# Performance work log

Measured on AMD Instinct MI355X. Metric: run time of the kernel, lower is better.

## Reference

```python
import jax, jax.numpy as jnp
import numpy as np

B, T, C = 256, 256, 147
BPM, H_DIM, NH = 32, 64, 4
HD = H_DIM // NH


def setup_inputs() -> dict:
    key = jax.random.key(0)
    ks = jax.random.split(key, 12)
    def lin(k, fan_in, fan_out):
        bound = 1.0 / np.sqrt(fan_in)
        kw, kb = jax.random.split(k)
        W = jax.random.uniform(kw, (fan_in, fan_out), jnp.float32, -bound, bound)
        b = jax.random.uniform(kb, (fan_out,), jnp.float32, -bound, bound)
        return W, b
    Wq, bq = lin(ks[0], C, H_DIM)
    Wk, bk = lin(ks[1], C, H_DIM)
    Wv, bv = lin(ks[2], C, H_DIM)
    Wb, bb = lin(ks[3], BPM, H_DIM)
    Wo, bo = lin(ks[4], H_DIM, C)
    pose = jax.random.normal(ks[5], (B, T, C), jnp.float32)
    bpm_emb = jax.random.normal(ks[6], (B, BPM), jnp.float32)
    return {"pose": pose, "bpm_emb": bpm_emb,
            "Wq": Wq, "bq": bq, "Wk": Wk, "bk": bk, "Wv": Wv, "bv": bv,
            "Wb": Wb, "bb": bb, "Wo": Wo, "bo": bo}


def reference(pose, bpm_emb, Wq, bq, Wk, bk, Wv, bv, Wb, bb, Wo, bo):
    Bb, Tt, Cc = pose.shape
    scale = HD ** -0.5
    # projections -> [B, H, T, hd]
    def split_heads(x):
        return x.reshape(Bb, Tt, NH, HD).transpose(0, 2, 1, 3)
    q = split_heads(pose @ Wq + bq)
    k = split_heads(pose @ Wk + bk)
    v = split_heads(pose @ Wv + bv)
    # bpm-conditioned key bias: [B, H, 1, hd]
    bpm_feat = (bpm_emb @ Wb + bb).reshape(Bb, 1, NH, HD).transpose(0, 2, 1, 3)
    k = k + bpm_feat
    # attention
    scores = jnp.einsum('bhqd,bhkd->bhqk', q, k) * scale
    attn = jax.nn.softmax(scores, axis=-1)
    out = jnp.einsum('bhqk,bhkd->bhqd', attn, v)
    out = out.transpose(0, 2, 1, 3).reshape(Bb, Tt, NH * HD)
    return out @ Wo + bo
```

## Files before the change

### kernel.cpp

```cpp
#include <hip/hip_runtime.h>

constexpr int kC = 147, kH = 64, kHD = 16, kBPM = 32;

typedef __attribute__((ext_vector_type(8)))  short bf16x8;
typedef __attribute__((ext_vector_type(4)))  float f32x4;
typedef __attribute__((ext_vector_type(16))) float f32x16;
typedef __attribute__((ext_vector_type(4)))  short s16x4;

__device__ __forceinline__ short f2bf(float f) {
    unsigned u = __builtin_bit_cast(unsigned, f);
    u += 0x7fffu + ((u >> 16) & 1u);
    return (short)(u >> 16);
}
#define MFMA16(a,b,c) __builtin_amdgcn_mfma_f32_16x16x32_bf16((a),(b),(c),0,0,0)
#define MFMA32(a,b,c) __builtin_amdgcn_mfma_f32_32x32x16_bf16((a),(b),(c),0,0,0)

#if __has_builtin(__builtin_amdgcn_exp2f)
  #define EXP2(x) __builtin_amdgcn_exp2f(x)
#else
  #define EXP2(x) __expf((x) * 0.6931471805599453f)
#endif
constexpr float kQScale = 0.25f * 1.4426950408889634f;

constexpr int QS  = 72;
constexpr int VS  = 264;
constexpr int PS  = 40;
constexpr int WSS = 168;
constexpr int WOS = 72;

__device__ __forceinline__ void stage_w_qkv(const float* __restrict__ W,
                                            float scale, short* Ws, int tid) {
    #pragma unroll
    for (int it = 0; it < 5; ++it) {
        const int i = it * 1024 + tid;
        const int c = i & 63, k = (i >> 6) * 2;
        const float v0 = (k     < kC) ? W[k * kH + c] * scale : 0.f;
        const float v1 = (k + 1 < kC) ? W[(k + 1) * kH + c] * scale : 0.f;
        const unsigned pack = (unsigned)(unsigned short)f2bf(v0)
                            | ((unsigned)(unsigned short)f2bf(v1) << 16);
        *(unsigned*)&Ws[c * WSS + (k ^ (((c >> 3) & 3) << 3))] = pack;
    }
}

__global__ __launch_bounds__(1024, 4) void fused_kernel(
    const float* __restrict__ pose, const float* __restrict__ bpm_emb,
    const float* __restrict__ Wq, const float* __restrict__ bq,
    const float* __restrict__ Wk, const float* __restrict__ bk,
    const float* __restrict__ Wv, const float* __restrict__ bv,
    const float* __restrict__ Wb, const float* __restrict__ bb,
    const float* __restrict__ Wo, const float* __restrict__ bo,
    float* __restrict__ out)
{
    __shared__ __align__(16) short qs[256 * QS];
    __shared__ __align__(16) short ks_[256 * QS];
    __shared__ __align__(16) short vt[kH * VS];
    __shared__ __align__(16) short WsPt[20480];
    __shared__ float l_s[16 * 64];
    __shared__ float bias_s[192];
    short* const Ws = WsPt;
    short* const Pt = WsPt;

    const int tid = threadIdx.x;
    const int w = tid >> 6, lane = tid & 63;
    const int ll = lane & 15, lq = lane >> 4;
    const int lm = lane & 31, lh = lane >> 5;
    const int b = blockIdx.x;
    const size_t pbase = (size_t)b * 256 * kC;

    bf16x8 pf[5];
    {
        const int row = w * 16 + ll;
        const float* prow = pose + pbase + (size_t)row * kC;
        #pragma unroll
        for (int ksp = 0; ksp < 5; ++ksp) {
            const int c0 = ksp * 32 + lq * 8;
            float v[8];
            if (c0 + 8 <= kC) {
                const float4 f0 = *(const float4*)(prow + c0);
                const float4 f1 = *(const float4*)(prow + c0 + 4);
                v[0]=f0.x; v[1]=f0.y; v[2]=f0.z; v[3]=f0.w;
                v[4]=f1.x; v[5]=f1.y; v[6]=f1.z; v[7]=f1.w;
            } else {
                #pragma unroll
                for (int e = 0; e < 8; ++e) v[e] = (c0 + e < kC) ? prow[c0 + e] : 0.f;
            }
            bf16x8 t;
            #pragma unroll
            for (int e = 0; e < 8; ++e) t[e] = f2bf(v[e]);
            pf[ksp] = t;
        }
    }
    if (tid < 192) {
        const int m = tid >> 6, c = tid & 63;
        float a = ((m == 0) ? bq : (m == 1) ? bk : bv)[c];
        if (m == 1) {
            a += bb[c];
            #pragma unroll
            for (int k2 = 0; k2 < kBPM; ++k2)
                a = fmaf(bpm_emb[b * kBPM + k2], Wb[k2 * kH + c], a);
        }
        if (m == 0) a *= kQScale;
        bias_s[tid] = a;
    }
    stage_w_qkv(Wq, kQScale, Ws, tid);
    __syncthreads();

    for (int m = 0; m < 3; ++m) {
        f32x4 acc[4];
        #pragma unroll
        for (int mt = 0; mt < 4; ++mt) acc[mt] = (f32x4){0.f,0.f,0.f,0.f};
        #pragma unroll
        for (int ksp = 0; ksp < 5; ++ksp)
            #pragma unroll
            for (int mt = 0; mt < 4; ++mt) {
                const int c = mt * 16 + ll;
                const int key = ((c >> 3) & 3) << 3;
                const bf16x8 wf = *(const bf16x8*)(Ws + c * WSS + ((ksp*32 + lq*8) ^ key));
                acc[mt] = MFMA16(wf, pf[ksp], acc[mt]);
            }
        __syncthreads();
        if (m == 0)      stage_w_qkv(Wk, 1.0f, Ws, tid);
        else if (m == 1) stage_w_qkv(Wv, 1.0f, Ws, tid);
        const int row = w * 16 + ll;
        #pragma unroll
        for (int mt = 0; mt < 4; ++mt) {
            const int c0 = mt * 16 + 4 * lq;
            const float4 bv4 = *(const float4*)&bias_s[m * kH + c0];
            if (m < 2) {
                s16x4 pk;
                pk[0] = f2bf(acc[mt][0] + bv4.x);
                pk[1] = f2bf(acc[mt][1] + bv4.y);
                pk[2] = f2bf(acc[mt][2] + bv4.z);
                pk[3] = f2bf(acc[mt][3] + bv4.w);
                *(s16x4*)((m == 0 ? qs : ks_) + row * QS + c0) = pk;
            } else {
                vt[(c0 + 0) * VS + row] = f2bf(acc[mt][0] + bv4.x);
                vt[(c0 + 1) * VS + row] = f2bf(acc[mt][1] + bv4.y);
                vt[(c0 + 2) * VS + row] = f2bf(acc[mt][2] + bv4.z);
                vt[(c0 + 3) * VS + row] = f2bf(acc[mt][3] + bv4.w);
            }
        }
        __syncthreads();
    }

    const int h = w & 3;
    const int q0 = (w >> 2) * 64;
    bf16x8 qf[2];
    #pragma unroll
    for (int s32 = 0; s32 < 2; ++s32)
        qf[s32] = *(const bf16x8*)(qs + (q0 + s32*32 + lm) * QS + h*16 + lh*8);

    f32x4 oacc[2][2];
    #pragma unroll
    for (int s32 = 0; s32 < 2; ++s32) {
        oacc[s32][0] = (f32x4){0.f,0.f,0.f,0.f};
        oacc[s32][1] = (f32x4){0.f,0.f,0.f,0.f};
    }
    float lp[2] = {0.f, 0.f};
    short* Pw = Pt + w * 32 * PS;
    const int wkey = ((lm >> 3) & 3) << 3;

    for (int jb = 0; jb < 8; ++jb) {
        const int j0 = jb * 32;
        const bf16x8 kf = *(const bf16x8*)(ks_ + (j0 + lm) * QS + h*16 + lh*8);
        const bf16x8 vf = *(const bf16x8*)(vt + (h*16 + ll) * VS + j0 + lq*8);
        #pragma unroll
        for (int s32 = 0; s32 < 2; ++s32) {
            const f32x16 z16 = {0.f,0.f,0.f,0.f,0.f,0.f,0.f,0.f,
                                0.f,0.f,0.f,0.f,0.f,0.f,0.f,0.f};
            const f32x16 s = MFMA32(kf, qf[s32], z16);
            float sum = 0.f;
            #pragma unroll
            for (int g = 0; g < 4; ++g) {
                const float p0 = EXP2(s[4*g + 0]);
                const float p1 = EXP2(s[4*g + 1]);
                const float p2 = EXP2(s[4*g + 2]);
                const float p3 = EXP2(s[4*g + 3]);
                sum += (p0 + p1) + (p2 + p3);
                s16x4 pk; pk[0] = f2bf(p0); pk[1] = f2bf(p1);
                pk[2] = f2bf(p2); pk[3] = f2bf(p3);
                *(s16x4*)(Pw + lm * PS + ((8*g + 4*lh) ^ wkey)) = pk;
            }
            lp[s32] += sum;
            #pragma unroll
            for (int half = 0; half < 2; ++half) {
                const int qp = half * 16 + ll;
                const int rkey = ((qp >> 3) & 3) << 3;
                const bf16x8 pfr = *(const bf16x8*)(Pw + qp * PS + ((lq*8) ^ rkey));
                oacc[s32][half] = MFMA16(vf, pfr, oacc[s32][half]);
            }
        }
    }
    #pragma unroll
    for (int s32 = 0; s32 < 2; ++s32) {
        const float l2 = lp[s32] + __shfl_xor(lp[s32], 32);
        if (lane < 32) l_s[w * 64 + s32 * 32 + lm] = l2;
    }
    #pragma unroll
    for (int s32 = 0; s32 < 2; ++s32)
        #pragma unroll
        for (int half = 0; half < 2; ++half) {
            const int qi = s32 * 32 + half * 16 + ll;
            const float inv = 1.f / l_s[w * 64 + qi];
            s16x4 pk;
            #pragma unroll
            for (int r = 0; r < 4; ++r) pk[r] = f2bf(oacc[s32][half][r] * inv);
            *(s16x4*)(qs + (q0 + qi) * QS + h*16 + 4*lq) = pk;
        }
    __syncthreads();

    #pragma unroll
    for (int it = 0; it < 5; ++it) {
        const int i = it * 1024 + tid;
        const int n = i % 160, k = (i / 160) * 2;
        const float v0 = (n < kC) ? Wo[k * kC + n] : 0.f;
        const float v1 = (n < kC) ? Wo[(k + 1) * kC + n] : 0.f;
        const unsigned pack = (unsigned)(unsigned short)f2bf(v0)
                            | ((unsigned)(unsigned short)f2bf(v1) << 16);
        *(unsigned*)&Ws[n * WOS + (k ^ (((n >> 3) & 3) << 3))] = pack;
    }
    __syncthreads();

    bf16x8 xf[2];
    #pragma unroll
    for (int k2 = 0; k2 < 2; ++k2)
        xf[k2] = *(const bf16x8*)(qs + (w*16 + ll) * QS + k2*32 + lq*8);

    f32x4 po[10];
    #pragma unroll
    for (int mt = 0; mt < 10; ++mt) po[mt] = (f32x4){0.f,0.f,0.f,0.f};
    #pragma unroll
    for (int k2 = 0; k2 < 2; ++k2)
        #pragma unroll
        for (int mt = 0; mt < 10; ++mt) {
            const int n = mt * 16 + ll;
            const int key = ((n >> 3) & 3) << 3;
            const bf16x8 wf = *(const bf16x8*)(Ws + n * WOS + ((k2*32 + lq*8) ^ key));
            po[mt] = MFMA16(wf, xf[k2], po[mt]);
        }
    {
        const int row = w * 16 + ll;
        float* orow = out + ((size_t)b * 256 + row) * kC;
        #pragma unroll
        for (int mt = 0; mt < 10; ++mt) {
            const int c0 = mt * 16 + 4 * lq;
            if (mt < 9) {
                const float4 bv4 = *(const float4*)(bo + c0);
                float4 o;
                o.x = po[mt][0] + bv4.x; o.y = po[mt][1] + bv4.y;
                o.z = po[mt][2] + bv4.z; o.w = po[mt][3] + bv4.w;
                *(float4*)(orow + c0) = o;
            } else {
                #pragma unroll
                for (int r = 0; r < 4; ++r) {
                    const int c = c0 + r;
                    if (c < kC) orow[c] = po[mt][r] + bo[c];
                }
            }
        }
    }
}

extern "C" void kernel_launch(void* const* d_in, const int* in_sizes, int n_in,
                              void* d_out, int out_size, void* d_ws, size_t ws_size,
                              hipStream_t stream) {
    const float* pose    = (const float*)d_in[0];
    const float* bpm_emb = (const float*)d_in[1];
    const float* Wq = (const float*)d_in[2];  const float* bq = (const float*)d_in[3];
    const float* Wk = (const float*)d_in[4];  const float* bk = (const float*)d_in[5];
    const float* Wv = (const float*)d_in[6];  const float* bv = (const float*)d_in[7];
    const float* Wb = (const float*)d_in[8];  const float* bb = (const float*)d_in[9];
    const float* Wo = (const float*)d_in[10]; const float* bo = (const float*)d_in[11];
    float* out = (float*)d_out;

    fused_kernel<<<256, 1024, 0, stream>>>(
        pose, bpm_emb, Wq, bq, Wk, bk, Wv, bv, Wb, bb, Wo, bo, out);
}
```

Baseline: 134.7 us.

## Double-buffer QKV weight staging, use packed bf16 converts, and interleave attention MFMA/softmax

Splits the shared weight buffer into two halves so the next projection weight is staged while the current one is consumed, which drops one barrier per projection. Replaces the software bf16 rounding with the hardware v_cvt_pk_bf16_f32 instruction. Reorders the attention inner loop so the second score MFMA overlaps the first P·V, adding s_setprio hints, and changes the weight-staging index maps for better coalescing. Shared memory use grows, which may lower occupancy, and the packed convert may round differently from the manual routine.

Measured after the change: 139.1 us. 1.03x slower.

```diff
diff --git a/kernel.cpp b/kernel.cpp
--- a/kernel.cpp
+++ b/kernel.cpp
@@ -1,16 +1,22 @@
 #include <hip/hip_runtime.h>
 
-constexpr int kC = 147, kH = 64, kHD = 16, kBPM = 32;
+constexpr int kC = 147, kH = 64, kBPM = 32;
 
 typedef __attribute__((ext_vector_type(8)))  short bf16x8;
 typedef __attribute__((ext_vector_type(4)))  float f32x4;
 typedef __attribute__((ext_vector_type(16))) float f32x16;
-typedef __attribute__((ext_vector_type(4)))  short s16x4;
+typedef __attribute__((ext_vector_type(2)))  unsigned u32x2;
+typedef __attribute__((ext_vector_type(4)))  unsigned u32x4;
 
 __device__ __forceinline__ short f2bf(float f) {
     unsigned u = __builtin_bit_cast(unsigned, f);
     u += 0x7fffu + ((u >> 16) & 1u);
     return (short)(u >> 16);
+}
+__device__ __forceinline__ unsigned cvt_pk(float lo, float hi) {
+    unsigned r;
+    asm("v_cvt_pk_bf16_f32 %0, %1, %2" : "=v"(r) : "v"(lo), "v"(hi));
+    return r;
 }
 #define MFMA16(a,b,c) __builtin_amdgcn_mfma_f32_16x16x32_bf16((a),(b),(c),0,0,0)
 #define MFMA32(a,b,c) __builtin_amdgcn_mfma_f32_32x32x16_bf16((a),(b),(c),0,0,0)
@@ -33,12 +39,11 @@
     #pragma unroll
     for (int it = 0; it < 5; ++it) {
         const int i = it * 1024 + tid;
-        const int c = i & 63, k = (i >> 6) * 2;
+        const int c = (i >> 4) & 63;
+        const int k = (it * 16 + (i & 15)) * 2;
         const float v0 = (k     < kC) ? W[k * kH + c] * scale : 0.f;
         const float v1 = (k + 1 < kC) ? W[(k + 1) * kH + c] * scale : 0.f;
-        const unsigned pack = (unsigned)(unsigned short)f2bf(v0)
-                            | ((unsigned)(unsigned short)f2bf(v1) << 16);
-        *(unsigned*)&Ws[c * WSS + (k ^ (((c >> 3) & 3) << 3))] = pack;
+        *(unsigned*)&Ws[c * WSS + (k ^ (((c >> 3) & 3) << 3))] = cvt_pk(v0, v1);
     }
 }
 
@@ -54,11 +59,10 @@
     __shared__ __align__(16) short qs[256 * QS];
     __shared__ __align__(16) short ks_[256 * QS];
     __shared__ __align__(16) short vt[kH * VS];
-    __shared__ __align__(16) short WsPt[20480];
+    __shared__ __align__(16) short Ws0[64 * WSS];
+    __shared__ __align__(16) short Ws1[64 * WSS];
     __shared__ float l_s[16 * 64];
     __shared__ float bias_s[192];
-    short* const Ws = WsPt;
-    short* const Pt = WsPt;
 
     const int tid = threadIdx.x;
     const int w = tid >> 6, lane = tid & 63;
@@ -84,10 +88,9 @@
                 #pragma unroll
                 for (int e = 0; e < 8; ++e) v[e] = (c0 + e < kC) ? prow[c0 + e] : 0.f;
             }
-            bf16x8 t;
-            #pragma unroll
-            for (int e = 0; e < 8; ++e) t[e] = f2bf(v[e]);
-            pf[ksp] = t;
+            const u32x4 t = { cvt_pk(v[0], v[1]), cvt_pk(v[2], v[3]),
+                              cvt_pk(v[4], v[5]), cvt_pk(v[6], v[7]) };
+            pf[ksp] = __builtin_bit_cast(bf16x8, t);
         }
     }
     if (tid < 192) {
@@ -102,10 +105,14 @@
         if (m == 0) a *= kQScale;
         bias_s[tid] = a;
     }
-    stage_w_qkv(Wq, kQScale, Ws, tid);
+    stage_w_qkv(Wq, kQScale, Ws0, tid);
     __syncthreads();
 
+    #pragma unroll
     for (int m = 0; m < 3; ++m) {
+        if (m == 0)      stage_w_qkv(Wk, 1.0f, Ws1, tid);
+        else if (m == 1) stage_w_qkv(Wv, 1.0f, Ws0, tid);
+        const short* R = (m == 1) ? Ws1 : Ws0;
         f32x4 acc[4];
         #pragma unroll
         for (int mt = 0; mt < 4; ++mt) acc[mt] = (f32x4){0.f,0.f,0.f,0.f};
@@ -115,24 +122,18 @@
             for (int mt = 0; mt < 4; ++mt) {
                 const int c = mt * 16 + ll;
                 const int key = ((c >> 3) & 3) << 3;
-                const bf16x8 wf = *(const bf16x8*)(Ws + c * WSS + ((ksp*32 + lq*8) ^ key));
+                const bf16x8 wf = *(const bf16x8*)(R + c * WSS + ((ksp*32 + lq*8) ^ key));
                 acc[mt] = MFMA16(wf, pf[ksp], acc[mt]);
             }
-        __syncthreads();
-        if (m == 0)      stage_w_qkv(Wk, 1.0f, Ws, tid);
-        else if (m == 1) stage_w_qkv(Wv, 1.0f, Ws, tid);
         const int row = w * 16 + ll;
         #pragma unroll
         for (int mt = 0; mt < 4; ++mt) {
             const int c0 = mt * 16 + 4 * lq;
             const float4 bv4 = *(const float4*)&bias_s[m * kH + c0];
             if (m < 2) {
-                s16x4 pk;
-                pk[0] = f2bf(acc[mt][0] + bv4.x);
-                pk[1] = f2bf(acc[mt][1] + bv4.y);
-                pk[2] = f2bf(acc[mt][2] + bv4.z);
-                pk[3] = f2bf(acc[mt][3] + bv4.w);
-                *(s16x4*)((m == 0 ? qs : ks_) + row * QS + c0) = pk;
+                const u32x2 pk = { cvt_pk(acc[mt][0] + bv4.x, acc[mt][1] + bv4.y),
+                                   cvt_pk(acc[mt][2] + bv4.z, acc[mt][3] + bv4.w) };
+                *(u32x2*)((m == 0 ? qs : ks_) + row * QS + c0) = pk;
             } else {
                 vt[(c0 + 0) * VS + row] = f2bf(acc[mt][0] + bv4.x);
                 vt[(c0 + 1) * VS + row] = f2bf(acc[mt][1] + bv4.y);
@@ -157,39 +158,80 @@
         oacc[s32][1] = (f32x4){0.f,0.f,0.f,0.f};
     }
     float lp[2] = {0.f, 0.f};
-    short* Pw = Pt + w * 32 * PS;
+    short* Pw = (w < 8) ? (Ws0 + w * 32 * PS) : (Ws1 + (w - 8) * 32 * PS);
     const int wkey = ((lm >> 3) & 3) << 3;
-
+    const f32x16 z16 = {0.f,0.f,0.f,0.f,0.f,0.f,0.f,0.f,
+                        0.f,0.f,0.f,0.f,0.f,0.f,0.f,0.f};
+
+    #pragma unroll 2
     for (int jb = 0; jb < 8; ++jb) {
         const int j0 = jb * 32;
         const bf16x8 kf = *(const bf16x8*)(ks_ + (j0 + lm) * QS + h*16 + lh*8);
         const bf16x8 vf = *(const bf16x8*)(vt + (h*16 + ll) * VS + j0 + lq*8);
-        #pragma unroll
-        for (int s32 = 0; s32 < 2; ++s32) {
-            const f32x16 z16 = {0.f,0.f,0.f,0.f,0.f,0.f,0.f,0.f,
-                                0.f,0.f,0.f,0.f,0.f,0.f,0.f,0.f};
-            const f32x16 s = MFMA32(kf, qf[s32], z16);
-            float sum = 0.f;
-            #pragma unroll
-            for (int g = 0; g < 4; ++g) {
-                const float p0 = EXP2(s[4*g + 0]);
-                const float p1 = EXP2(s[4*g + 1]);
-                const float p2 = EXP2(s[4*g + 2]);
-                const float p3 = EXP2(s[4*g + 3]);
-                sum += (p0 + p1) + (p2 + p3);
-                s16x4 pk; pk[0] = f2bf(p0); pk[1] = f2bf(p1);
-                pk[2] = f2bf(p2); pk[3] = f2bf(p3);
-                *(s16x4*)(Pw + lm * PS + ((8*g + 4*lh) ^ wkey)) = pk;
-            }
-            lp[s32] += sum;
-            #pragma unroll
-            for (int half = 0; half < 2; ++half) {
-                const int qp = half * 16 + ll;
-                const int rkey = ((qp >> 3) & 3) << 3;
-                const bf16x8 pfr = *(const bf16x8*)(Pw + qp * PS + ((lq*8) ^ rkey));
-                oacc[s32][half] = MFMA16(vf, pfr, oacc[s32][half]);
-            }
-        }
+
+        __builtin_amdgcn_s_setprio(1);
+        const f32x16 s0 = MFMA32(kf, qf[0], z16);
+        __builtin_amdgcn_s_setprio(0);
+        float sum0 = 0.f;
+        unsigned u0[8];
+        #pragma unroll
+        for (int g = 0; g < 4; ++g) {
+            const float p0 = EXP2(s0[4*g + 0]);
+            const float p1 = EXP2(s0[4*g + 1]);
+            const float p2 = EXP2(s0[4*g + 2]);
+            const float p3 = EXP2(s0[4*g + 3]);
+            sum0 += (p0 + p1) + (p2 + p3);
+            u0[2*g]   = cvt_pk(p0, p1);
+            u0[2*g+1] = cvt_pk(p2, p3);
+        }
+        lp[0] += sum0;
+        #pragma unroll
+        for (int g = 0; g < 4; ++g) {
+            const u32x2 pk = { u0[2*g], u0[2*g+1] };
+            *(u32x2*)(Pw + lm * PS + ((8*g + 4*lh) ^ wkey)) = pk;
+        }
+
+        __builtin_amdgcn_s_setprio(1);
+        const f32x16 s1 = MFMA32(kf, qf[1], z16);
+        __builtin_amdgcn_s_setprio(0);
+        float sum1 = 0.f;
+        unsigned u1[8];
+        #pragma unroll
+        for (int g = 0; g < 4; ++g) {
+            const float p0 = EXP2(s1[4*g + 0]);
+            const float p1 = EXP2(s1[4*g + 1]);
+            const float p2 = EXP2(s1[4*g + 2]);
+            const float p3 = EXP2(s1[4*g + 3]);
+            sum1 += (p0 + p1) + (p2 + p3);
+            u1[2*g]   = cvt_pk(p0, p1);
+            u1[2*g+1] = cvt_pk(p2, p3);
+        }
+        lp[1] += sum1;
+
+        __builtin_amdgcn_s_setprio(1);
+        #pragma unroll
+        for (int hf = 0; hf < 2; ++hf) {
+            const int qp = hf * 16 + ll;
+            const int rkey = ((qp >> 3) & 3) << 3;
+            const bf16x8 pfr = *(const bf16x8*)(Pw + qp * PS + ((lq*8) ^ rkey));
+            oacc[0][hf] = MFMA16(vf, pfr, oacc[0][hf]);
+        }
+        __builtin_amdgcn_s_setprio(0);
+
+        #pragma unroll
+        for (int g = 0; g < 4; ++g) {
+            const u32x2 pk = { u1[2*g], u1[2*g+1] };
+            *(u32x2*)(Pw + lm * PS + ((8*g + 4*lh) ^ wkey)) = pk;
+        }
+        __builtin_amdgcn_s_setprio(1);
+        #pragma unroll
+        for (int hf = 0; hf < 2; ++hf) {
+            const int qp = hf * 16 + ll;
+            const int rkey = ((qp >> 3) & 3) << 3;
+            const bf16x8 pfr = *(const bf16x8*)(Pw + qp * PS + ((lq*8) ^ rkey));
+            oacc[1][hf] = MFMA16(vf, pfr, oacc[1][hf]);
+        }
+        __builtin_amdgcn_s_setprio(0);
     }
     #pragma unroll
     for (int s32 = 0; s32 < 2; ++s32) {
@@ -199,25 +241,23 @@
     #pragma unroll
     for (int s32 = 0; s32 < 2; ++s32)
         #pragma unroll
-        for (int half = 0; half < 2; ++half) {
-            const int qi = s32 * 32 + half * 16 + ll;
+        for (int hf = 0; hf < 2; ++hf) {
+            const int qi = s32 * 32 + hf * 16 + ll;
             const float inv = 1.f / l_s[w * 64 + qi];
-            s16x4 pk;
-            #pragma unroll
-            for (int r = 0; r < 4; ++r) pk[r] = f2bf(oacc[s32][half][r] * inv);
-            *(s16x4*)(qs + (q0 + qi) * QS + h*16 + 4*lq) = pk;
+            const u32x2 pk = { cvt_pk(oacc[s32][hf][0] * inv, oacc[s32][hf][1] * inv),
+                               cvt_pk(oacc[s32][hf][2] * inv, oacc[s32][hf][3] * inv) };
+            *(u32x2*)(qs + (q0 + qi) * QS + h*16 + 4*lq) = pk;
         }
     __syncthreads();
 
     #pragma unroll
     for (int it = 0; it < 5; ++it) {
         const int i = it * 1024 + tid;
-        const int n = i % 160, k = (i / 160) * 2;
+        const int n = i >> 5, k = (i & 31) * 2;
         const float v0 = (n < kC) ? Wo[k * kC + n] : 0.f;
         const float v1 = (n < kC) ? Wo[(k + 1) * kC + n] : 0.f;
-        const unsigned pack = (unsigned)(unsigned short)f2bf(v0)
-                            | ((unsigned)(unsigned short)f2bf(v1) << 16);
-        *(unsigned*)&Ws[n * WOS + (k ^ (((n >> 3) & 3) << 3))] = pack;
+        short* base = (n < 144) ? (Ws0 + n * WOS) : (Ws1 + (n - 144) * WOS);
+        *(unsigned*)&base[k ^ (((n >> 3) & 3) << 3)] = cvt_pk(v0, v1);
     }
     __syncthreads();
 
@@ -235,7 +275,8 @@
         for (int mt = 0; mt < 10; ++mt) {
             const int n = mt * 16 + ll;
             const int key = ((n >> 3) & 3) << 3;
-            const bf16x8 wf = *(const bf16x8*)(Ws + n * WOS + ((k2*32 + lq*8) ^ key));
+            const short* base = (mt < 9) ? (Ws0 + n * WOS) : (Ws1 + (n - 144) * WOS);
+            const bf16x8 wf = *(const bf16x8*)(base + ((k2*32 + lq*8) ^ key));
             po[mt] = MFMA16(wf, xf[k2], po[mt]);
         }
     {
```
